# Optimization experiments

Measured on AMD Instinct MI355X. Metric: run time of the kernel, lower is better.

Reference implementation:

```python
import jax, jax.numpy as jnp
import numpy as np

N = 50000   # nodes
E = 1600000 # edges
D = 128     # feature dim (in = hidden = 128)


def setup_inputs() -> dict:
    key = jax.random.key(0)
    k1, k2, k3, k4 = jax.random.split(key, 4)
    scale = 1.0 / np.sqrt(D)
    return {
        "x": jax.random.normal(k1, (N, D), jnp.float32),
        "edge_index": jax.random.randint(k2, (2, E), 0, N, dtype=jnp.int32),
        "W0": jax.random.normal(k3, (D, D), jnp.float32) * scale,
        "b0": jnp.zeros((D,), jnp.float32),
        "W1": jax.random.normal(k4, (D, D), jnp.float32) * scale,
        "b1": jnp.zeros((D,), jnp.float32),
    }


def _gcn_norm(edge_index, num_nodes):
    # Add self-loops, compute symmetric normalization D^-1/2 A_hat D^-1/2.
    loop = jnp.arange(num_nodes, dtype=edge_index.dtype)
    src = jnp.concatenate([edge_index[0], loop])
    dst = jnp.concatenate([edge_index[1], loop])
    deg = jax.ops.segment_sum(jnp.ones_like(dst, jnp.float32), dst,
                              num_segments=num_nodes)
    dinv = jnp.where(deg > 0, jax.lax.rsqrt(deg), 0.0)
    norm = dinv[dst] * dinv[src]  # [E+N]
    return src, dst, norm


def _gcn_layer(x, src, dst, norm, W, b, num_nodes):
    h = x @ W                                  # [N, D]
    msg = h[src] * norm[:, None]               # gather + scale  [E+N, D]
    out = jax.ops.segment_sum(msg, dst, num_segments=num_nodes)  # scatter-add
    return out + b


def reference(x, edge_index, W0, b0, W1, b1):
    num_nodes = x.shape[0]
    src, dst, norm = _gcn_norm(edge_index, num_nodes)
    # forward loops over the first k=2 convs, ReLU after each (as in source)
    x = jax.nn.relu(_gcn_layer(x, src, dst, norm, W0, b0, num_nodes))
    x = jax.nn.relu(_gcn_layer(x, src, dst, norm, W1, b1, num_nodes))
    return x
```

## Files before the change

kernel.cpp:

```cpp
#include <hip/hip_runtime.h>
#include <hip/hip_bf16.h>

#define D 128
#define CHUNK 8192
#define SPAN_CAP 768


typedef __attribute__((ext_vector_type(8))) short short8;
typedef __attribute__((ext_vector_type(4))) float floatx4;

static __device__ inline unsigned int f2bf(float f) {
    unsigned int u = __float_as_uint(f);
    return (u + 0x7FFFu + ((u >> 16) & 1u)) >> 16;
}
static __device__ inline float bflo(unsigned int u) { return __uint_as_float(u << 16); }
static __device__ inline float bfhi(unsigned int u) { return __uint_as_float(u & 0xFFFF0000u); }

__global__ __launch_bounds__(256) void k01_swz_hist(const float* __restrict__ W0,
                                                    const float* __restrict__ W1,
                                                    short8* __restrict__ whi0, short8* __restrict__ wlo0,
                                                    short8* __restrict__ whi1, short8* __restrict__ wlo1,
                                                    const int* __restrict__ dst,
                                                    int* __restrict__ blockhist, int E_) {
    __shared__ int h[256];
    const int tid = threadIdx.x;
    if (blockIdx.x < 16) {
        int gid = blockIdx.x * 256 + tid;
        const float* W = (gid < 2048) ? W0 : W1;
        short8* whi = (gid < 2048) ? whi0 : whi1;
        short8* wlo = (gid < 2048) ? wlo0 : wlo1;
        int t2 = gid & 2047;
        int t = t2 >> 8, q = (t2 >> 6) & 3, lane = t2 & 63;
        short8 hi, lo;
        #pragma unroll
        for (int j = 0; j < 8; ++j) {
            int k = q * 32 + (lane >> 4) * 8 + j;
            int n = t * 16 + (lane & 15);
            float w = W[k * D + n];
            unsigned int hh = f2bf(w);
            hi[j] = (short)hh;
            lo[j] = (short)f2bf(w - __uint_as_float(hh << 16));
        }
        whi[t2] = hi;
        wlo[t2] = lo;
    } else {
        const int b = blockIdx.x - 16;
        h[tid] = 0;
        __syncthreads();
        const int e0 = b * CHUNK;
        const int e1 = min(E_, e0 + CHUNK);
        for (int e = e0 + tid; e < e1; e += 256)
            atomicAdd(&h[dst[e] >> 8], 1);
        __syncthreads();
        blockhist[b * 256 + tid] = h[tid];
    }
}

__global__ __launch_bounds__(256) void k23_scan_scatter(const int* __restrict__ blockhist,
                                                        const int* __restrict__ dst,
                                                        const int* __restrict__ src,
                                                        int* __restrict__ bucket_offs,
                                                        unsigned int* __restrict__ buf,
                                                        int NB, int NBUK, int E_) {
    __shared__ int s[256];
    __shared__ int c[256];
    const int myb = blockIdx.x, tid = threadIdx.x;
    int total = 0, prefix = 0;
    #pragma unroll 4
    for (int b2 = 0; b2 < NB; ++b2) {
        int t = blockhist[b2 * 256 + tid];
        total += t;
        prefix += (b2 < myb) ? t : 0;
    }
    s[tid] = total;
    __syncthreads();
    #pragma unroll
    for (int off = 1; off < 256; off <<= 1) {
        int x = (tid >= off) ? s[tid - off] : 0;
        __syncthreads();
        s[tid] += x;
        __syncthreads();
    }
    int bstart = s[tid] - total;
    if (myb == 0) {
        if (tid < NBUK) bucket_offs[tid] = bstart;
        if (tid == 0) bucket_offs[NBUK] = E_;
    }
    c[tid] = bstart + prefix;
    __syncthreads();

    const int e0 = myb * CHUNK;
    const int e1 = min(E_, e0 + CHUNK);
    for (int e = e0 + tid; e < e1; e += 256) {
        int v = dst[e];
        int sdx = src[e];
        int pos = atomicAdd(&c[v >> 8], 1);
        buf[pos] = (unsigned int)sdx | ((unsigned int)(v & 255) << 16);
    }
}

__global__ __launch_bounds__(256) void k4_bucket(const unsigned int* __restrict__ buf,
                                                 const int* __restrict__ bucket_offs,
                                                 int* __restrict__ offs,
                                                 float* __restrict__ dinv,
                                                 int* __restrict__ col, int N_, int E_) {
    __shared__ int h[256];
    __shared__ int s[256];
    __shared__ int c[256];
    const int beta = blockIdx.x, tid = threadIdx.x;
    const int start = bucket_offs[beta];
    const int end   = bucket_offs[beta + 1];

    h[tid] = 0;
    __syncthreads();
    for (int e = start + tid; e < end; e += 256)
        atomicAdd(&h[(buf[e] >> 16) & 255], 1);
    __syncthreads();

    int deg = h[tid];
    s[tid] = deg;
    __syncthreads();
    #pragma unroll
    for (int off = 1; off < 256; off <<= 1) {
        int x = (tid >= off) ? s[tid - off] : 0;
        __syncthreads();
        s[tid] += x;
        __syncthreads();
    }
    int excl = s[tid] - deg;

    int v0 = beta * 256 + tid;
    if (v0 < N_) {
        offs[v0] = start + excl;
        dinv[v0] = rsqrtf((float)(deg + 1));
    }
    if (beta == 0 && tid == 0) offs[N_] = E_;
    c[tid] = start + excl;
    __syncthreads();

    for (int e = start + tid; e < end; e += 256) {
        unsigned int p = buf[e];
        int pos = atomicAdd(&c[(p >> 16) & 255], 1);
        col[pos] = (int)(p & 0xFFFFu);
    }
}

__global__ __launch_bounds__(256) void gemm_mfma(const float* __restrict__ A,
                                                 const short8* __restrict__ whi,
                                                 const short8* __restrict__ wlo,
                                                 const float* __restrict__ dinv,
                                                 unsigned int* __restrict__ Gu, int nrows) {
    __shared__ float tileT[128][65];

    const int tid  = threadIdx.x;
    const int wave = tid >> 6, lane = tid & 63;
    const int m = lane & 15, quad = lane >> 4;
    const int rowInBlk = wave * 16;
    const int arow = min(blockIdx.x * 64 + rowInBlk + m, nrows - 1);
    const float* Ap = A + (size_t)arow * D + quad * 8;

    floatx4 acc[8];
    #pragma unroll
    for (int t = 0; t < 8; ++t) acc[t] = (floatx4){0.f, 0.f, 0.f, 0.f};

    #pragma unroll
    for (int q = 0; q < 4; ++q) {
        float4 a0 = *(const float4*)(Ap + q * 32);
        float4 a1 = *(const float4*)(Ap + q * 32 + 4);
        float av[8] = {a0.x, a0.y, a0.z, a0.w, a1.x, a1.y, a1.z, a1.w};
        short8 ahi, alo;
        #pragma unroll
        for (int j = 0; j < 8; ++j) {
            unsigned int h = f2bf(av[j]);
            ahi[j] = (short)h;
            alo[j] = (short)f2bf(av[j] - __uint_as_float(h << 16));
        }
        #pragma unroll
        for (int t = 0; t < 8; ++t) {
            short8 bh = whi[(t * 4 + q) * 64 + lane];
            short8 bl = wlo[(t * 4 + q) * 64 + lane];
            acc[t] = __builtin_amdgcn_mfma_f32_16x16x32_bf16(ahi, bh, acc[t], 0, 0, 0);
            acc[t] = __builtin_amdgcn_mfma_f32_16x16x32_bf16(alo, bh, acc[t], 0, 0, 0);
            acc[t] = __builtin_amdgcn_mfma_f32_16x16x32_bf16(ahi, bl, acc[t], 0, 0, 0);
        }
    }

    #pragma unroll
    for (int t = 0; t < 8; ++t)
        #pragma unroll
        for (int r = 0; r < 4; ++r)
            tileT[t * 16 + m][rowInBlk + quad * 4 + r] = acc[t][r];
    __syncthreads();

    const int orow = tid >> 2, seg = tid & 3;
    const int grow = blockIdx.x * 64 + orow;
    if (grow < nrows) {
        float s = dinv[grow];
        const int p = seg >> 1;
        unsigned int* Gp = Gu + ((size_t)(p * nrows + grow)) * 32 + (seg & 1) * 16;
        #pragma unroll
        for (int i = 0; i < 4; ++i) {
            int c0 = seg * 32 + i * 8;
            uint4 o4;
            o4.x = f2bf(tileT[c0 + 0][orow] * s) | (f2bf(tileT[c0 + 1][orow] * s) << 16);
            o4.y = f2bf(tileT[c0 + 2][orow] * s) | (f2bf(tileT[c0 + 3][orow] * s) << 16);
            o4.z = f2bf(tileT[c0 + 4][orow] * s) | (f2bf(tileT[c0 + 5][orow] * s) << 16);
            o4.w = f2bf(tileT[c0 + 6][orow] * s) | (f2bf(tileT[c0 + 7][orow] * s) << 16);
            ((uint4*)Gp)[i] = o4;
        }
    }
}

__global__ __launch_bounds__(256) void aggregate_kernel(const unsigned int* __restrict__ Gu,
                                                        const int* __restrict__ offs,
                                                        const int* __restrict__ col,
                                                        const float* __restrict__ dinv,
                                                        const float* __restrict__ bias,
                                                        float* __restrict__ out, int nnodes,
                                                        int ngroups) {
    __shared__ int scol[SPAN_CAP];
    __shared__ int soffs[9];
    const int bid   = blockIdx.x;
    const int xcd   = bid & 7;
    const int plane = xcd >> 2;
    const int i     = (bid >> 3) * 4 + (xcd & 3);
    if (i >= ngroups) return;
    const int tid   = threadIdx.x;
    const int node0 = i * 8;

    if (tid < 9) soffs[tid] = offs[min(node0 + tid, nnodes)];
    __syncthreads();
    const int s0   = soffs[0];
    const int span = soffs[8] - s0;
    const bool lds_ok = (span <= SPAN_CAP);
    if (lds_ok) {
        for (int k = tid; k < span; k += 256) scol[k] = col[s0 + k];
    }
    __syncthreads();

    const int lane = tid & 31;
    const int node = node0 + (tid >> 5);
    if (node >= nnodes) return;
    const unsigned int* P = Gu + (size_t)plane * nnodes * 32;

    unsigned int su = P[(size_t)node * 32 + lane];
    float ax = bflo(su), ay = bfhi(su);

    const int s = soffs[tid >> 5];
    const int e = soffs[(tid >> 5) + 1];
    int idx = s;

    if (lds_ok) {
        const int b0 = s - s0;
        int k = 0;
        const int deg = e - s;
        for (; k + 8 <= deg; k += 8) {
            int j0 = scol[b0 + k + 0], j1 = scol[b0 + k + 1], j2 = scol[b0 + k + 2], j3 = scol[b0 + k + 3];
            int j4 = scol[b0 + k + 4], j5 = scol[b0 + k + 5], j6 = scol[b0 + k + 6], j7 = scol[b0 + k + 7];
            unsigned int u0 = P[(size_t)j0 * 32 + lane];
            unsigned int u1 = P[(size_t)j1 * 32 + lane];
            unsigned int u2 = P[(size_t)j2 * 32 + lane];
            unsigned int u3 = P[(size_t)j3 * 32 + lane];
            unsigned int u4 = P[(size_t)j4 * 32 + lane];
            unsigned int u5 = P[(size_t)j5 * 32 + lane];
            unsigned int u6 = P[(size_t)j6 * 32 + lane];
            unsigned int u7 = P[(size_t)j7 * 32 + lane];
            ax += ((bflo(u0) + bflo(u1)) + (bflo(u2) + bflo(u3))) +
                  ((bflo(u4) + bflo(u5)) + (bflo(u6) + bflo(u7)));
            ay += ((bfhi(u0) + bfhi(u1)) + (bfhi(u2) + bfhi(u3))) +
                  ((bfhi(u4) + bfhi(u5)) + (bfhi(u6) + bfhi(u7)));
        }
        for (; k + 4 <= deg; k += 4) {
            int j0 = scol[b0 + k + 0], j1 = scol[b0 + k + 1], j2 = scol[b0 + k + 2], j3 = scol[b0 + k + 3];
            unsigned int u0 = P[(size_t)j0 * 32 + lane];
            unsigned int u1 = P[(size_t)j1 * 32 + lane];
            unsigned int u2 = P[(size_t)j2 * 32 + lane];
            unsigned int u3 = P[(size_t)j3 * 32 + lane];
            ax += (bflo(u0) + bflo(u1)) + (bflo(u2) + bflo(u3));
            ay += (bfhi(u0) + bfhi(u1)) + (bfhi(u2) + bfhi(u3));
        }
        for (; k < deg; ++k) {
            unsigned int u = P[(size_t)scol[b0 + k] * 32 + lane];
            ax += bflo(u);
            ay += bfhi(u);
        }
    } else {
        for (; idx + 4 <= e; idx += 4) {
            int j0 = col[idx + 0], j1 = col[idx + 1], j2 = col[idx + 2], j3 = col[idx + 3];
            unsigned int u0 = P[(size_t)j0 * 32 + lane];
            unsigned int u1 = P[(size_t)j1 * 32 + lane];
            unsigned int u2 = P[(size_t)j2 * 32 + lane];
            unsigned int u3 = P[(size_t)j3 * 32 + lane];
            ax += (bflo(u0) + bflo(u1)) + (bflo(u2) + bflo(u3));
            ay += (bfhi(u0) + bfhi(u1)) + (bfhi(u2) + bfhi(u3));
        }
        for (; idx < e; ++idx) {
            unsigned int u = P[(size_t)col[idx] * 32 + lane];
            ax += bflo(u);
            ay += bfhi(u);
        }
    }

    float dv = dinv[node];
    float2 bb = ((const float2*)bias)[plane * 32 + lane];
    float2 o;
    o.x = fmaxf(fmaf(dv, ax, bb.x), 0.f);
    o.y = fmaxf(fmaf(dv, ay, bb.y), 0.f);
    ((float2*)out)[(size_t)node * 64 + plane * 32 + lane] = o;
}

extern "C" void kernel_launch(void* const* d_in, const int* in_sizes, int n_in,
                              void* d_out, int out_size, void* d_ws, size_t ws_size,
                              hipStream_t stream) {
    const float* x    = (const float*)d_in[0];
    const int*   edge = (const int*)d_in[1];
    const float* W0   = (const float*)d_in[2];
    const float* b0   = (const float*)d_in[3];
    const float* W1   = (const float*)d_in[4];
    const float* b1   = (const float*)d_in[5];
    float* out = (float*)d_out;

    const int N_ = in_sizes[0] / D;
    const int E_ = in_sizes[1] / 2;
    const int* srcp = edge;
    const int* dstp = edge + E_;

    const int NB   = (E_ + CHUNK - 1) / CHUNK;
    const int NBUK = (N_ + 255) >> 8;

    char* p = (char*)d_ws;
    auto carve = [&](size_t bytes) { char* q = p; p += (bytes + 255) & ~(size_t)255; return q; };
    int*          blockhist = (int*)          carve((size_t)NB * 256 * 4);
    int*          buck_offs = (int*)          carve((size_t)(NBUK + 1) * 4);
    int*          offs      = (int*)          carve((size_t)(N_ + 1) * 4);
    float*        dinv      = (float*)        carve((size_t)N_ * 4);
    unsigned int* buf       = (unsigned int*) carve((size_t)E_ * 4);
    int*          col       = (int*)          carve((size_t)E_ * 4);
    unsigned int* gu        = (unsigned int*) carve((size_t)N_ * 64 * 4);
    short8*       whi0      = (short8*)       carve(2048 * 16);
    short8*       wlo0      = (short8*)       carve(2048 * 16);
    short8*       whi1      = (short8*)       carve(2048 * 16);
    short8*       wlo1      = (short8*)       carve(2048 * 16);

    k01_swz_hist   <<<16 + NB, 256, 0, stream>>>(W0, W1, whi0, wlo0, whi1, wlo1,
                                                 dstp, blockhist, E_);
    k23_scan_scatter<<<NB,     256, 0, stream>>>(blockhist, dstp, srcp, buck_offs, buf,
                                                 NB, NBUK, E_);
    k4_bucket      <<<NBUK,    256, 0, stream>>>(buf, buck_offs, offs, dinv, col, N_, E_);

    const int gmb = (N_ + 63) / 64;
    const int ngroups = (N_ + 7) / 8;
    const int agrid   = ((ngroups + 3) / 4) * 8;

    gemm_mfma       <<<gmb,   256, 0, stream>>>(x, whi0, wlo0, dinv, gu, N_);
    aggregate_kernel<<<agrid, 256, 0, stream>>>(gu, offs, col, dinv, b0, out, N_, ngroups);
    gemm_mfma       <<<gmb,   256, 0, stream>>>(out, whi1, wlo1, dinv, gu, N_);
    aggregate_kernel<<<agrid, 256, 0, stream>>>(gu, offs, col, dinv, b1, out, N_, ngroups);
}
```

Measured before the change: 259.1 us.

## Fuse CSR build kernels into one cooperative kernel with grid syncs

Merges the weight-swizzle/histogram, scan/scatter and bucket-sort kernels into a single cooperative launch that uses grid.sync between phases. CHUNK is doubled so fewer histogram blocks are needed, and the grid is sized to max(16+NB, NBUK). This removes two kernel launch gaps in exchange for grid-wide barriers, a grid of only about 196 blocks, and half as many blocks doing the histogram and scatter phases, each handling more edges.

```diff
diff --git a/kernel.cpp b/kernel.cpp
--- a/kernel.cpp
+++ b/kernel.cpp
@@ -1,8 +1,11 @@
 #include <hip/hip_runtime.h>
 #include <hip/hip_bf16.h>
+#include <hip/hip_cooperative_groups.h>
+
+namespace cg = cooperative_groups;
 
 #define D 128
-#define CHUNK 8192
+#define CHUNK 16384
 #define SPAN_CAP 768
 
 
@@ -16,16 +19,28 @@
 static __device__ inline float bflo(unsigned int u) { return __uint_as_float(u << 16); }
 static __device__ inline float bfhi(unsigned int u) { return __uint_as_float(u & 0xFFFF0000u); }
 
-__global__ __launch_bounds__(256) void k01_swz_hist(const float* __restrict__ W0,
-                                                    const float* __restrict__ W1,
-                                                    short8* __restrict__ whi0, short8* __restrict__ wlo0,
-                                                    short8* __restrict__ whi1, short8* __restrict__ wlo1,
-                                                    const int* __restrict__ dst,
-                                                    int* __restrict__ blockhist, int E_) {
+__global__ __launch_bounds__(256) void build_all(const float* __restrict__ W0,
+                                                 const float* __restrict__ W1,
+                                                 short8* __restrict__ whi0, short8* __restrict__ wlo0,
+                                                 short8* __restrict__ whi1, short8* __restrict__ wlo1,
+                                                 const int* __restrict__ dst,
+                                                 const int* __restrict__ src,
+                                                 int* __restrict__ blockhist,
+                                                 int* __restrict__ bucket_offs,
+                                                 unsigned int* __restrict__ buf,
+                                                 int* __restrict__ offs,
+                                                 float* __restrict__ dinv,
+                                                 int* __restrict__ col,
+                                                 int NB, int NBUK, int N_, int E_) {
+    cg::grid_group grid = cg::this_grid();
     __shared__ int h[256];
+    __shared__ int s[256];
+    __shared__ int c[256];
     const int tid = threadIdx.x;
-    if (blockIdx.x < 16) {
-        int gid = blockIdx.x * 256 + tid;
+    const int bx  = blockIdx.x;
+
+    if (bx < 16) {
+        int gid = bx * 256 + tid;
         const float* W = (gid < 2048) ? W0 : W1;
         short8* whi = (gid < 2048) ? whi0 : whi1;
         short8* wlo = (gid < 2048) ? wlo0 : wlo1;
@@ -43,8 +58,8 @@
         }
         whi[t2] = hi;
         wlo[t2] = lo;
-    } else {
-        const int b = blockIdx.x - 16;
+    } else if (bx < 16 + NB) {
+        const int b = bx - 16;
         h[tid] = 0;
         __syncthreads();
         const int e0 = b * CHUNK;
@@ -54,94 +69,80 @@
         __syncthreads();
         blockhist[b * 256 + tid] = h[tid];
     }
-}
-
-__global__ __launch_bounds__(256) void k23_scan_scatter(const int* __restrict__ blockhist,
-                                                        const int* __restrict__ dst,
-                                                        const int* __restrict__ src,
-                                                        int* __restrict__ bucket_offs,
-                                                        unsigned int* __restrict__ buf,
-                                                        int NB, int NBUK, int E_) {
-    __shared__ int s[256];
-    __shared__ int c[256];
-    const int myb = blockIdx.x, tid = threadIdx.x;
-    int total = 0, prefix = 0;
-    #pragma unroll 4
-    for (int b2 = 0; b2 < NB; ++b2) {
-        int t = blockhist[b2 * 256 + tid];
-        total += t;
-        prefix += (b2 < myb) ? t : 0;
-    }
-    s[tid] = total;
-    __syncthreads();
-    #pragma unroll
-    for (int off = 1; off < 256; off <<= 1) {
-        int x = (tid >= off) ? s[tid - off] : 0;
-        __syncthreads();
-        s[tid] += x;
-        __syncthreads();
-    }
-    int bstart = s[tid] - total;
-    if (myb == 0) {
-        if (tid < NBUK) bucket_offs[tid] = bstart;
-        if (tid == 0) bucket_offs[NBUK] = E_;
-    }
-    c[tid] = bstart + prefix;
-    __syncthreads();
-
-    const int e0 = myb * CHUNK;
-    const int e1 = min(E_, e0 + CHUNK);
-    for (int e = e0 + tid; e < e1; e += 256) {
-        int v = dst[e];
-        int sdx = src[e];
-        int pos = atomicAdd(&c[v >> 8], 1);
-        buf[pos] = (unsigned int)sdx | ((unsigned int)(v & 255) << 16);
-    }
-}
-
-__global__ __launch_bounds__(256) void k4_bucket(const unsigned int* __restrict__ buf,
-                                                 const int* __restrict__ bucket_offs,
-                                                 int* __restrict__ offs,
-                                                 float* __restrict__ dinv,
-                                                 int* __restrict__ col, int N_, int E_) {
-    __shared__ int h[256];
-    __shared__ int s[256];
-    __shared__ int c[256];
-    const int beta = blockIdx.x, tid = threadIdx.x;
-    const int start = bucket_offs[beta];
-    const int end   = bucket_offs[beta + 1];
-
-    h[tid] = 0;
-    __syncthreads();
-    for (int e = start + tid; e < end; e += 256)
-        atomicAdd(&h[(buf[e] >> 16) & 255], 1);
-    __syncthreads();
-
-    int deg = h[tid];
-    s[tid] = deg;
-    __syncthreads();
-    #pragma unroll
-    for (int off = 1; off < 256; off <<= 1) {
-        int x = (tid >= off) ? s[tid - off] : 0;
-        __syncthreads();
-        s[tid] += x;
-        __syncthreads();
-    }
-    int excl = s[tid] - deg;
-
-    int v0 = beta * 256 + tid;
-    if (v0 < N_) {
-        offs[v0] = start + excl;
-        dinv[v0] = rsqrtf((float)(deg + 1));
-    }
-    if (beta == 0 && tid == 0) offs[N_] = E_;
-    c[tid] = start + excl;
-    __syncthreads();
-
-    for (int e = start + tid; e < end; e += 256) {
-        unsigned int p = buf[e];
-        int pos = atomicAdd(&c[(p >> 16) & 255], 1);
-        col[pos] = (int)(p & 0xFFFFu);
+    grid.sync();
+
+    if (bx < NB) {
+        int total = 0, prefix = 0;
+        #pragma unroll 4
+        for (int b2 = 0; b2 < NB; ++b2) {
+            int t = blockhist[b2 * 256 + tid];
+            total += t;
+            prefix += (b2 < bx) ? t : 0;
+        }
+        s[tid] = total;
+        __syncthreads();
+        #pragma unroll
+        for (int off = 1; off < 256; off <<= 1) {
+            int x = (tid >= off) ? s[tid - off] : 0;
+            __syncthreads();
+            s[tid] += x;
+            __syncthreads();
+        }
+        int bstart = s[tid] - total;
+        if (bx == 0) {
+            if (tid < NBUK) bucket_offs[tid] = bstart;
+            if (tid == 0) bucket_offs[NBUK] = E_;
+        }
+        c[tid] = bstart + prefix;
+        __syncthreads();
+
+        const int e0 = bx * CHUNK;
+        const int e1 = min(E_, e0 + CHUNK);
+        for (int e = e0 + tid; e < e1; e += 256) {
+            int v = dst[e];
+            int sdx = src[e];
+            int pos = atomicAdd(&c[v >> 8], 1);
+            buf[pos] = (unsigned int)sdx | ((unsigned int)(v & 255) << 16);
+        }
+    }
+    grid.sync();
+
+    if (bx < NBUK) {
+        const int start = bucket_offs[bx];
+        const int end   = bucket_offs[bx + 1];
+
+        h[tid] = 0;
+        __syncthreads();
+        for (int e = start + tid; e < end; e += 256)
+            atomicAdd(&h[(buf[e] >> 16) & 255], 1);
+        __syncthreads();
+
+        int deg = h[tid];
+        s[tid] = deg;
+        __syncthreads();
+        #pragma unroll
+        for (int off = 1; off < 256; off <<= 1) {
+            int x = (tid >= off) ? s[tid - off] : 0;
+            __syncthreads();
+            s[tid] += x;
+            __syncthreads();
+        }
+        int excl = s[tid] - deg;
+
+        int v0 = bx * 256 + tid;
+        if (v0 < N_) {
+            offs[v0] = start + excl;
+            dinv[v0] = rsqrtf((float)(deg + 1));
+        }
+        if (bx == 0 && tid == 0) offs[N_] = E_;
+        c[tid] = start + excl;
+        __syncthreads();
+
+        for (int e = start + tid; e < end; e += 256) {
+            unsigned int p = buf[e];
+            int pos = atomicAdd(&c[(p >> 16) & 255], 1);
+            col[pos] = (int)(p & 0xFFFFu);
+        }
     }
 }
 
@@ -342,11 +343,20 @@
     short8*       whi1      = (short8*)       carve(2048 * 16);
     short8*       wlo1      = (short8*)       carve(2048 * 16);
 
-    k01_swz_hist   <<<16 + NB, 256, 0, stream>>>(W0, W1, whi0, wlo0, whi1, wlo1,
-                                                 dstp, blockhist, E_);
-    k23_scan_scatter<<<NB,     256, 0, stream>>>(blockhist, dstp, srcp, buck_offs, buf,
-                                                 NB, NBUK, E_);
-    k4_bucket      <<<NBUK,    256, 0, stream>>>(buf, buck_offs, offs, dinv, col, N_, E_);
+    int bgrid = 16 + NB;
+    if (NBUK > bgrid) bgrid = NBUK;
+    {
+        void* args[] = {
+            (void*)&W0, (void*)&W1,
+            (void*)&whi0, (void*)&wlo0, (void*)&whi1, (void*)&wlo1,
+            (void*)&dstp, (void*)&srcp,
+            (void*)&blockhist, (void*)&buck_offs,
+            (void*)&buf, (void*)&offs, (void*)&dinv, (void*)&col,
+            (void*)&NB, (void*)&NBUK, (void*)&N_, (void*)&E_
+        };
+        hipLaunchCooperativeKernel((void*)build_all, dim3(bgrid), dim3(256),
+                                   args, 0, stream);
+    }
 
     const int gmb = (N_ + 63) / 64;
     const int ngroups = (N_ + 7) / 8;
```

New measurement: 336.2 us. +29.8%, slower.
